# Optimization experiments

Measured on AMD Instinct MI355X. Metric: run time of the kernel, lower is better.

The kernel has to match this reference:

```python
import jax, jax.numpy as jnp
import numpy as np


def _cif_cmat(w_seq):
    """Integrate-and-fire assignment matrix for one sequence.
    w_seq: [T] sigmoid weights. Returns [T, T+1] (T+1 is a static upper
    bound on the number of fired output frames)."""
    T = w_seq.shape[0]
    cols = jnp.arange(T + 1)

    def step(carry, w):
        acc, k = carry
        fire = acc + w > 1.0
        on_k = (cols == k).astype(w.dtype)
        on_k1 = (cols == k + 1).astype(w.dtype)
        row_fire = on_k * (1.0 - acc) / w + on_k1 * (acc + w - 1.0) / w
        row = jnp.where(fire, row_fire, on_k)
        acc_new = jnp.where(fire, jnp.zeros_like(acc), acc + w)  # original resets acc to 0
        k_new = jnp.where(fire, k + 1, k)
        return (acc_new, k_new), row

    init = (jnp.zeros((), w_seq.dtype), jnp.zeros((), jnp.int32))
    _, rows = jax.lax.scan(step, init, w_seq)
    return rows  # [T, T+1]


def setup_inputs() -> dict:
    key = jax.random.key(0)
    k1, k2, k3 = jax.random.split(key, 3)
    B, T, D = 8, 2000, 512
    feat = jax.random.normal(k1, (B, T, D), dtype=jnp.float32)
    hlens = jax.random.randint(k2, (B,), 0, T).astype(jnp.int32)
    W = jax.random.normal(k3, (D,), dtype=jnp.float32) * (1.0 / np.sqrt(D))
    b = jnp.zeros((1,), dtype=jnp.float32)
    return {"feat": feat, "hlens": hlens, "W": W, "b": b}


def reference(feat, hlens, W, b):
    # weight = sigmoid(Linear(feat))  -> [B, T]
    weight = jax.nn.sigmoid(jnp.einsum("btd,d->bt", feat, W) + b[0])
    hlens_new = jnp.ceil(jnp.sum(weight, axis=1)).astype(jnp.int32)
    # sequential integrate-and-fire scan, vmapped over batch -> [B, T, T+1]
    weight_cmat = jax.lax.stop_gradient(jax.vmap(_cif_cmat)(weight))
    weight_mat = weight[:, :, None] * weight_cmat        # [B, T, M]
    feat_new = jnp.einsum("btd,btm->bmd", feat, weight_mat)  # [B, M, D]
    return feat_new, hlens_new
```

## Files before the change

### kernel.cpp

```cpp
#include <hip/hip_runtime.h>
#include <math.h>

#define BATCH 8
#define TLEN 2000
#define DIM 512
#define MLEN (TLEN + 1)
#define NTH 1024
#define NWORD 32
#define MAXLVL 11

__global__ __launch_bounds__(256) void weight_kernel(
    const float* __restrict__ feat, const float* __restrict__ W,
    const float* __restrict__ bias, float* __restrict__ weight) {
  int gwave = (blockIdx.x * 256 + threadIdx.x) >> 6;
  int lane  = threadIdx.x & 63;
  if (gwave >= BATCH * TLEN) return;
  const float4* f4 = (const float4*)feat + (size_t)gwave * (DIM / 4) + lane * 2;
  const float4* w4 = (const float4*)W + lane * 2;
  float4 a0 = f4[0], a1 = f4[1];
  float4 b0 = w4[0], b1 = w4[1];
  float s = a0.x * b0.x + a0.y * b0.y + a0.z * b0.z + a0.w * b0.w +
            a1.x * b1.x + a1.y * b1.y + a1.z * b1.z + a1.w * b1.w;
#pragma unroll
  for (int off = 32; off > 0; off >>= 1) s += __shfl_xor(s, off, 64);
  if (lane == 0) {
    float x = s + bias[0];
    weight[gwave] = 1.0f / (1.0f + expf(-x));
  }
}

__global__ __launch_bounds__(NTH) void scan_kernel(
    const float* __restrict__ weight, float* __restrict__ hlens_out,
    float2* __restrict__ c01G, int2* __restrict__ AB) {
  int b = blockIdx.x;
  int tid = threadIdx.x;
  int lane = tid & 63, wid = tid >> 6;

  __shared__ float w_s[TLEN];
  __shared__ float S_s[TLEN];
  __shared__ float wtot[16];
  __shared__ unsigned short Ga_s[MLEN];
  __shared__ unsigned short Gb_s[MLEN];
  __shared__ unsigned short F_s[2048];
  __shared__ unsigned long long mask_s[NWORD];
  __shared__ int lastw_s[NWORD];
  __shared__ int done_lv[MAXLVL];
  __shared__ int K_s;

  const float* wrow = weight + b * TLEN;
  int base = tid * 2;
  float w0 = 0.f, w1 = 0.f;
  if (base < TLEN) {
    float2 v = *(const float2*)(wrow + base);
    w0 = v.x; w1 = v.y;
  }
  float mysum = w0 + w1;
  float sc = mysum;
#pragma unroll
  for (int d = 1; d < 64; d <<= 1) {
    float o = __shfl_up(sc, d, 64);
    if (lane >= d) sc += o;
  }
  if (lane == 63) wtot[wid] = sc;
  if (tid < NWORD) mask_s[tid] = 0ull;
  if (tid < MAXLVL) done_lv[tid] = 1;
  __syncthreads();
  float woff = 0.f;
  for (int j = 0; j < wid; j++) woff += wtot[j];
  float excl = woff + (sc - mysum);
  if (base < TLEN) {
    w_s[base] = w0; w_s[base + 1] = w1;
    S_s[base] = excl + w0;
    S_s[base + 1] = excl + w0 + w1;
  }
  if (tid == 0) {
    float tot = 0.f;
    for (int j = 0; j < 16; j++) tot += wtot[j];
    hlens_out[b] = ceilf(tot);
  }
  __syncthreads();

  {
    int l0 = tid + 1, r0 = TLEN;  float tg0 = S_s[tid] + 1.0f;
    int s1v = tid + 1024;
    bool has1 = (s1v < TLEN);
    int l1 = has1 ? s1v + 1 : TLEN, r1 = TLEN;
    float tg1 = has1 ? S_s[s1v] + 1.0f : 0.f;
    bool has2 = (tid == 0);
    int l2 = 0, r2 = has2 ? TLEN : 0;
#pragma unroll
    for (int step = 0; step < MAXLVL; step++) {
      if (l0 < r0) { int m = (l0 + r0) >> 1; if (S_s[m] > tg0) r0 = m; else l0 = m + 1; }
      if (l1 < r1) { int m = (l1 + r1) >> 1; if (S_s[m] > tg1) r1 = m; else l1 = m + 1; }
      if (l2 < r2) { int m = (l2 + r2) >> 1; if (S_s[m] > 1.0f) r2 = m; else l2 = m + 1; }
    }
    Ga_s[tid] = (unsigned short)l0;
    if (has1) Ga_s[s1v] = (unsigned short)l1;
    F_s[tid] = (unsigned short)TLEN;
    F_s[tid + 1024] = (unsigned short)TLEN;
    if (tid == 0) {
      Ga_s[TLEN] = (unsigned short)TLEN;
      F_s[0] = (unsigned short)l2;
    }
  }
  __syncthreads();

  {
    unsigned short* cur = Ga_s;
    unsigned short* nxt = Gb_s;
    int flen = 1;
    for (int lvl = 0; lvl < MAXLVL; lvl++) {
      int s0 = tid, s1v = tid + 1024;
      int g20 = (int)cur[cur[s0]];
      int g21 = (s1v <= TLEN) ? (int)cur[cur[s1v]] : TLEN;
      int i0 = tid, i1 = tid + 1024;
      int nv0 = -1, nv1 = -1;
      if (i0 < flen) nv0 = (int)cur[F_s[i0]];
      if (i1 < flen) nv1 = (int)cur[F_s[i1]];
      nxt[s0] = (unsigned short)g20;
      if (s1v <= TLEN) nxt[s1v] = (unsigned short)g21;
      if (i0 < flen) { F_s[flen + i0] = (unsigned short)nv0; if (nv0 < TLEN) done_lv[lvl] = 0; }
      if (i1 < flen) { F_s[flen + i1] = (unsigned short)nv1; if (nv1 < TLEN) done_lv[lvl] = 0; }
      __syncthreads();
      flen <<= 1;
      unsigned short* t = cur; cur = nxt; nxt = t;
      if (done_lv[lvl]) break;
    }
  }

  {
    int t0v = (int)F_s[tid];
    int t1v = (int)F_s[tid + 1024];
    if (t0v < TLEN) atomicOr(&mask_s[t0v >> 6], 1ull << (t0v & 63));
    if (t1v < TLEN) atomicOr(&mask_s[t1v >> 6], 1ull << (t1v & 63));
  }
  __syncthreads();
  if (tid == 0) {
    int last = -1, cnt = 0;
    for (int wd = 0; wd < NWORD; wd++) {
      lastw_s[wd] = last;
      unsigned long long m = mask_s[wd];
      cnt += __popcll(m);
      if (m) last = wd * 64 + 63 - __clzll(m);
    }
    K_s = cnt;
  }
  __syncthreads();
  int K = K_s;

#pragma unroll
  for (int it = 0; it < 2; it++) {
    int t = tid + it * 1024;
    if (t >= TLEN) continue;
    unsigned long long wd = mask_s[t >> 6];
    int bit = t & 63;
    unsigned long long below = wd & ((1ull << bit) - 1ull);
    int pf = below ? ((t & ~63) + 63 - __clzll(below)) : lastw_s[t >> 6];
    float Spf = (pf >= 0) ? S_s[pf] : 0.f;
    float accb = ((t > 0) ? S_s[t - 1] : 0.f) - Spf;
    bool fire = (wd >> bit) & 1ull;
    float c0 = fire ? (1.0f - accb) : w_s[t];
    float c1 = (S_s[t] - Spf) - 1.0f;
    c01G[b * TLEN + t] = float2{c0, c1};
  }

#pragma unroll
  for (int it = 0; it < 2; it++) {
    int m = tid + it * 1024;
    if (m >= MLEN) continue;
    int af = (m == 0) ? 0 : ((m <= K) ? (int)F_s[m - 1] : 0x7fffffff);
    int bl = (m < K) ? (int)F_s[m] : ((m == K) ? TLEN - 1 : -1);
    AB[(size_t)b * MLEN + m] = int2{af, bl};
  }
}

__global__ __launch_bounds__(256) void gather_kernel(
    const float* __restrict__ feat, const float2* __restrict__ c01G,
    const int2* __restrict__ AB, float* __restrict__ out) {
  int bm = (blockIdx.x * 256 + threadIdx.x) >> 6;
  int lane = threadIdx.x & 63;
  if (bm >= BATCH * MLEN) return;
  int b = bm / MLEN, m = bm % MLEN;
  int2 ab = AB[(size_t)bm];
  int a = ab.x, e = ab.y;
  int afire = (m > 0) ? a : -1;
  float4 acc0 = {0.f, 0.f, 0.f, 0.f};
  float4 acc1 = {0.f, 0.f, 0.f, 0.f};
  const float4* f4 = (const float4*)feat + (size_t)b * TLEN * (DIM / 4) + lane * 2;
  const float2* crow = c01G + b * TLEN;
  for (int t = a; t <= e; t++) {
    float2 c01 = crow[t];
    float c = (t == afire) ? c01.y : c01.x;
    const float4* fr = f4 + (size_t)t * (DIM / 4);
    float4 fa = fr[0], fb = fr[1];
    acc0.x += c * fa.x; acc0.y += c * fa.y; acc0.z += c * fa.z; acc0.w += c * fa.w;
    acc1.x += c * fb.x; acc1.y += c * fb.y; acc1.z += c * fb.z; acc1.w += c * fb.w;
  }
  float4* orow = (float4*)out + (size_t)bm * (DIM / 4) + lane * 2;
  orow[0] = acc0;
  orow[1] = acc1;
}

extern "C" void kernel_launch(void* const* d_in, const int* in_sizes, int n_in,
                              void* d_out, int out_size, void* d_ws, size_t ws_size,
                              hipStream_t stream) {
  const float* feat = (const float*)d_in[0];
  const float* W    = (const float*)d_in[2];
  const float* bias = (const float*)d_in[3];

  float* out       = (float*)d_out;
  float* feat_new  = out;
  float* hlens_out = out + (size_t)BATCH * MLEN * DIM;

  char* ws = (char*)d_ws;
  float*  weight = (float*)ws;
  float2* c01    = (float2*)(ws + 64000);
  int2*   AB     = (int2*)(ws + 192000);

  weight_kernel<<<(BATCH * TLEN) / 4, 256, 0, stream>>>(feat, W, bias, weight);
  scan_kernel<<<BATCH, NTH, 0, stream>>>(weight, hlens_out, c01, AB);
  int nframes = BATCH * MLEN;
  gather_kernel<<<(nframes + 3) / 4, 256, 0, stream>>>(feat, c01, AB, feat_new);
}
```

Baseline: 102.5 us.

## Compute frame endpoint coefficients per output frame instead of per-timestep coefficient table

Drops the bitmask-of-fire-positions pass, the serial single-thread prefix over mask words, and the per-timestep c0/c1 table. The scan kernel now finds K by locating the first sentinel in the fire list, and for each output frame stores only its start and end indices plus the two boundary coefficients in an int4. The gather kernel reads the raw sigmoid weights for interior timesteps. This removes a serial step and a global table write in the scan kernel, at the cost of an extra branch per timestep in the gather loop and a wider per-frame descriptor.

```diff
diff --git a/kernel.cpp b/kernel.cpp
--- a/kernel.cpp
+++ b/kernel.cpp
@@ -6,7 +6,6 @@
 #define DIM 512
 #define MLEN (TLEN + 1)
 #define NTH 1024
-#define NWORD 32
 #define MAXLVL 11
 
 __global__ __launch_bounds__(256) void weight_kernel(
@@ -31,7 +30,7 @@
 
 __global__ __launch_bounds__(NTH) void scan_kernel(
     const float* __restrict__ weight, float* __restrict__ hlens_out,
-    float2* __restrict__ c01G, int2* __restrict__ AB) {
+    int4* __restrict__ AB) {
   int b = blockIdx.x;
   int tid = threadIdx.x;
   int lane = tid & 63, wid = tid >> 6;
@@ -42,8 +41,6 @@
   __shared__ unsigned short Ga_s[MLEN];
   __shared__ unsigned short Gb_s[MLEN];
   __shared__ unsigned short F_s[2048];
-  __shared__ unsigned long long mask_s[NWORD];
-  __shared__ int lastw_s[NWORD];
   __shared__ int done_lv[MAXLVL];
   __shared__ int K_s;
 
@@ -62,7 +59,6 @@
     if (lane >= d) sc += o;
   }
   if (lane == 63) wtot[wid] = sc;
-  if (tid < NWORD) mask_s[tid] = 0ull;
   if (tid < MAXLVL) done_lv[tid] = 1;
   __syncthreads();
   float woff = 0.f;
@@ -128,69 +124,68 @@
     }
   }
 
-  {
-    int t0v = (int)F_s[tid];
-    int t1v = (int)F_s[tid + 1024];
-    if (t0v < TLEN) atomicOr(&mask_s[t0v >> 6], 1ull << (t0v & 63));
-    if (t1v < TLEN) atomicOr(&mask_s[t1v >> 6], 1ull << (t1v & 63));
-  }
-  __syncthreads();
-  if (tid == 0) {
-    int last = -1, cnt = 0;
-    for (int wd = 0; wd < NWORD; wd++) {
-      lastw_s[wd] = last;
-      unsigned long long m = mask_s[wd];
-      cnt += __popcll(m);
-      if (m) last = wd * 64 + 63 - __clzll(m);
-    }
-    K_s = cnt;
+#pragma unroll
+  for (int it = 0; it < 2; it++) {
+    int k = tid + it * 1024;
+    if ((int)F_s[k] == TLEN && (k == 0 || (int)F_s[k - 1] < TLEN)) K_s = k;
   }
   __syncthreads();
   int K = K_s;
-
-#pragma unroll
-  for (int it = 0; it < 2; it++) {
-    int t = tid + it * 1024;
-    if (t >= TLEN) continue;
-    unsigned long long wd = mask_s[t >> 6];
-    int bit = t & 63;
-    unsigned long long below = wd & ((1ull << bit) - 1ull);
-    int pf = below ? ((t & ~63) + 63 - __clzll(below)) : lastw_s[t >> 6];
-    float Spf = (pf >= 0) ? S_s[pf] : 0.f;
-    float accb = ((t > 0) ? S_s[t - 1] : 0.f) - Spf;
-    bool fire = (wd >> bit) & 1ull;
-    float c0 = fire ? (1.0f - accb) : w_s[t];
-    float c1 = (S_s[t] - Spf) - 1.0f;
-    c01G[b * TLEN + t] = float2{c0, c1};
-  }
 
 #pragma unroll
   for (int it = 0; it < 2; it++) {
     int m = tid + it * 1024;
     if (m >= MLEN) continue;
-    int af = (m == 0) ? 0 : ((m <= K) ? (int)F_s[m - 1] : 0x7fffffff);
-    int bl = (m < K) ? (int)F_s[m] : ((m == K) ? TLEN - 1 : -1);
-    AB[(size_t)b * MLEN + m] = int2{af, bl};
+    int a, e;
+    float cL = 0.f, cR = 0.f;
+    if (m == 0) {
+      a = 0;
+      if (K > 0) {
+        e = (int)F_s[0];
+        cR = 1.0f - ((e > 0) ? S_s[e - 1] : 0.f);
+      } else {
+        e = TLEN - 1;
+        cR = w_s[TLEN - 1];
+      }
+    } else if (m <= K) {
+      int f1 = (int)F_s[m - 1];
+      float Sp0 = (m >= 2) ? S_s[(int)F_s[m - 2]] : 0.f;
+      a = f1;
+      cL = S_s[f1] - Sp0 - 1.0f;
+      if (m < K) {
+        e = (int)F_s[m];
+        cR = 1.0f - (S_s[e - 1] - S_s[f1]);
+      } else {
+        e = TLEN - 1;
+        cR = w_s[TLEN - 1];
+      }
+    } else {
+      a = 0x7fffffff; e = -1;
+    }
+    int4 pk;
+    pk.x = a; pk.y = e;
+    pk.z = __float_as_int(cL);
+    pk.w = __float_as_int(cR);
+    AB[(size_t)b * MLEN + m] = pk;
   }
 }
 
 __global__ __launch_bounds__(256) void gather_kernel(
-    const float* __restrict__ feat, const float2* __restrict__ c01G,
-    const int2* __restrict__ AB, float* __restrict__ out) {
+    const float* __restrict__ feat, const float* __restrict__ weight,
+    const int4* __restrict__ AB, float* __restrict__ out) {
   int bm = (blockIdx.x * 256 + threadIdx.x) >> 6;
   int lane = threadIdx.x & 63;
   if (bm >= BATCH * MLEN) return;
   int b = bm / MLEN, m = bm % MLEN;
-  int2 ab = AB[(size_t)bm];
+  int4 ab = AB[(size_t)bm];
   int a = ab.x, e = ab.y;
-  int afire = (m > 0) ? a : -1;
+  float cL = __int_as_float(ab.z), cR = __int_as_float(ab.w);
   float4 acc0 = {0.f, 0.f, 0.f, 0.f};
   float4 acc1 = {0.f, 0.f, 0.f, 0.f};
   const float4* f4 = (const float4*)feat + (size_t)b * TLEN * (DIM / 4) + lane * 2;
-  const float2* crow = c01G + b * TLEN;
+  const float* wrow = weight + b * TLEN;
   for (int t = a; t <= e; t++) {
-    float2 c01 = crow[t];
-    float c = (t == afire) ? c01.y : c01.x;
+    float c = (t == a && m > 0) ? cL : ((t == e) ? cR : wrow[t]);
     const float4* fr = f4 + (size_t)t * (DIM / 4);
     float4 fa = fr[0], fb = fr[1];
     acc0.x += c * fa.x; acc0.y += c * fa.y; acc0.z += c * fa.z; acc0.w += c * fa.w;
@@ -213,12 +208,11 @@
   float* hlens_out = out + (size_t)BATCH * MLEN * DIM;
 
   char* ws = (char*)d_ws;
-  float*  weight = (float*)ws;
-  float2* c01    = (float2*)(ws + 64000);
-  int2*   AB     = (int2*)(ws + 192000);
+  float* weight = (float*)ws;
+  int4*  AB     = (int4*)(ws + 64000);
 
   weight_kernel<<<(BATCH * TLEN) / 4, 256, 0, stream>>>(feat, W, bias, weight);
-  scan_kernel<<<BATCH, NTH, 0, stream>>>(weight, hlens_out, c01, AB);
+  scan_kernel<<<BATCH, NTH, 0, stream>>>(weight, hlens_out, AB);
   int nframes = BATCH * MLEN;
-  gather_kernel<<<(nframes + 3) / 4, 256, 0, stream>>>(feat, c01, AB, feat_new);
-}
+  gather_kernel<<<(nframes + 3) / 4, 256, 0, stream>>>(feat, weight, AB, feat_new);
+}
```

Result: no change. 100.6 us (median of 2 runs) (-1.9%).
